# Kernel tuning notes

Measured on AMD Instinct MI355X. Metric: run time of the kernel, lower is better.

## Reference

```python
import jax, jax.numpy as jnp
import numpy as np

NUM_C = 100
DIM_S = 128
SIZE_M = 64
EMB = 128
MAX_CODE_LEN = 128
NODE_COUNT = 10000
PATH_COUNT = 10000
B, L = 16, 128


def setup_inputs() -> dict:
    key = jax.random.key(0)
    ks = jax.random.split(key, 24)
    def nrm(k, shape, fan):
        return jax.random.normal(k, shape, jnp.float32) * np.float32(np.sqrt(2.0 / fan))
    code = jax.random.randint(ks[0], (B, L, NUM_C * 2 + MAX_CODE_LEN * 3), 0, 10000)
    q = jax.random.randint(ks[1], (B, L), 0, NUM_C)
    r = jax.random.randint(ks[2], (B, L), 0, 2 * NUM_C)
    return {
        "code": code, "q": q, "r": r,
        "embed_nodes": nrm(ks[3], (NODE_COUNT + 2, EMB), EMB),
        "embed_paths": nrm(ks[4], (PATH_COUNT + 2, EMB), EMB),
        "W_pt": nrm(ks[5], (3 * EMB, 3 * EMB), 3 * EMB), "b_pt": jnp.zeros((3 * EMB,), jnp.float32),
        "W_att": nrm(ks[6], (3 * EMB, 1), 3 * EMB), "b_att": jnp.zeros((1,), jnp.float32),
        "k_emb": nrm(ks[7], (NUM_C + 1, DIM_S), DIM_S),
        "Mk": nrm(ks[8], (SIZE_M, DIM_S), DIM_S),
        "Mv0": nrm(ks[9], (SIZE_M, DIM_S), DIM_S),
        "v_emb": nrm(ks[10], (NUM_C * 2 + 2, DIM_S), DIM_S),
        "W_e": nrm(ks[11], (4 * DIM_S, DIM_S), 4 * DIM_S), "b_e": jnp.zeros((DIM_S,), jnp.float32),
        "W_a": nrm(ks[12], (4 * DIM_S, DIM_S), 4 * DIM_S), "b_a": jnp.zeros((DIM_S,), jnp.float32),
        "W_f": nrm(ks[13], (2 * DIM_S, DIM_S), 2 * DIM_S), "b_f": jnp.zeros((DIM_S,), jnp.float32),
        "W_p": nrm(ks[14], (DIM_S, 10), DIM_S), "b_p": jnp.zeros((10,), jnp.float32),
    }


def reference(code, q, r, embed_nodes, embed_paths, W_pt, b_pt, W_att, b_att,
              k_emb, Mk, Mv0, v_emb, W_e, b_e, W_a, b_a, W_f, b_f, W_p, b_p):
    bsz = code.shape[0]
    k = k_emb[q]                                    # [B,L,D]
    vr = v_emb[r]                                   # [B,L,D]
    # code2vec path triples: [B,L,MAX_CODE_LEN,3] = (start, path, end)
    c2v = code[:, :, NUM_C * 2:].reshape(bsz, code.shape[1], MAX_CODE_LEN, 3)
    full = jnp.concatenate([embed_nodes[c2v[..., 0]],
                            embed_nodes[c2v[..., 2]],
                            embed_paths[c2v[..., 1]]], axis=3)   # [B,L,P,3E]
    tr = jnp.tanh(full @ W_pt + b_pt)
    cw = tr @ W_att + b_att                          # [B,L,P,1]
    attn = jax.nn.softmax(cw, axis=1)                # faithful: softmax over seq dim (dim=1)
    code_vec = jnp.sum(full * attn, axis=2)          # [B,L,3E]
    v = jnp.concatenate([vr, code_vec], axis=2)      # [B,L,4D]
    w = jax.nn.softmax(k @ Mk.T, axis=-1)            # [B,L,M]
    e = jax.nn.sigmoid(v @ W_e + b_e)                # [B,L,D]
    a = jnp.tanh(v @ W_a + b_a)                      # [B,L,D]
    Mvt0 = jnp.broadcast_to(Mv0, (bsz,) + Mv0.shape) # [B,M,D]

    def step(Mvt, inp):
        et, at, wt = inp                             # [B,D],[B,D],[B,M]
        read = jnp.einsum('bm,bmd->bd', wt, Mvt)     # read pre-update memory (Mv[:, :-1])
        Mvt = Mvt * (1.0 - wt[:, :, None] * et[:, None, :]) + wt[:, :, None] * at[:, None, :]
        return Mvt, read

    _, reads = jax.lax.scan(step, Mvt0,
                            (e.transpose(1, 0, 2), a.transpose(1, 0, 2), w.transpose(1, 0, 2)))
    read = reads.transpose(1, 0, 2)                  # [B,L,D]
    f = jnp.tanh(jnp.concatenate([read, k], axis=-1) @ W_f + b_f)
    # dropout is identity in eval mode
    return jax.nn.sigmoid(f @ W_p + b_p)             # [B,L,10]
```

## Files before the change

kernel.cpp:

```cpp
#include <hip/hip_runtime.h>


typedef unsigned char u8;
typedef unsigned short u16;
typedef unsigned int u32;
typedef __attribute__((ext_vector_type(8))) short short8;
typedef __attribute__((ext_vector_type(4))) float f32x4;
typedef __attribute__((ext_vector_type(2))) float f32x2;

#define DEV __device__ __forceinline__
#define LOG2E 1.4426950408889634f
#define KSCALE 2.8853900817779268f

DEV u16 f2b(float f) {
    union { float f; u32 i; } v; v.f = f;
    u32 x = v.i;
    u32 r = (x + 0x7FFFu + ((x >> 16) & 1u)) >> 16;
    return (u16)r;
}
DEV float nexp(float x) { return __builtin_amdgcn_exp2f(x * LOG2E); }
DEV float nrcp(float x) { return __builtin_amdgcn_rcpf(x); }
DEV float fast_tanh(float x) {
    return 1.f - 2.f * nrcp(1.f + __builtin_amdgcn_exp2f(x * (2.f * LOG2E)));
}
DEV float sigmoidf_(float x) { return nrcp(1.f + __builtin_amdgcn_exp2f(-x * LOG2E)); }
DEV f32x2 d8(u32 x, bool hi) {
    return hi ? __builtin_amdgcn_cvt_pk_f32_fp8((int)x, true)
              : __builtin_amdgcn_cvt_pk_f32_fp8((int)x, false);
}
DEV u8 e8(float x) {
    return (u8)(__builtin_amdgcn_cvt_pk_fp8_f32(x, x, 0, false) & 0xFF);
}

__global__ void k_conv(const float* __restrict__ EN, const float* __restrict__ EP,
                       const float* __restrict__ Wpt, const float* __restrict__ We,
                       const float* __restrict__ Wa, const float* __restrict__ Wf,
                       const float* __restrict__ Wp,
                       const float* __restrict__ Kemb, const float* __restrict__ Mk,
                       u16* __restrict__ ENb, u16* __restrict__ EPb,
                       u8* __restrict__ EN8, u8* __restrict__ EP8,
                       u16* __restrict__ Wt, u16* __restrict__ WeaT,
                       u16* __restrict__ WfT, u16* __restrict__ WpT,
                       float* __restrict__ wsmall) {
    if (blockIdx.x >= 2048) {
        int wv = threadIdx.x >> 6, lane = threadIdx.x & 63;
        int row = (blockIdx.x - 2048) * 4 + wv;
        if (row >= 101) return;
        float lg = 0.f;
        for (int k = 0; k < 128; k += 8) {
            float mk8[8];
#pragma unroll
            for (int u = 0; u < 8; u++) mk8[u] = Mk[lane * 128 + k + u];
#pragma unroll
            for (int u = 0; u < 8; u++) lg = fmaf(Kemb[row * 128 + k + u], mk8[u], lg);
        }
        float mx = lg;
#pragma unroll
        for (int off = 32; off; off >>= 1) mx = fmaxf(mx, __shfl_xor(mx, off, 64));
        float ex = nexp(lg - mx);
        float sum = ex;
#pragma unroll
        for (int off = 32; off; off >>= 1) sum += __shfl_xor(sum, off, 64);
        wsmall[row * 64 + lane] = ex * nrcp(sum);
        return;
    }
    const int NEH = 10002 * 64;
    const int T0 = 2 * NEH;
    const int T1 = T0 + 147456;
    const int T2 = T1 + 65536;
    const int T2b = T2 + 65536;
    const int T3 = T2b + 32768;
    const int T4 = T3 + 2048;
    for (int i = blockIdx.x * blockDim.x + threadIdx.x; i < T4; i += 2048 * blockDim.x) {
        if (i < NEH) {
            float a = EN[2 * i], b = EN[2 * i + 1];
            ((u32*)ENb)[i] = ((u32)f2b(b) << 16) | f2b(a);
            ((u16*)EN8)[i] = (u16)__builtin_amdgcn_cvt_pk_fp8_f32(a, b, 0, false);
        } else if (i < T0) {
            int j = i - NEH;
            float a = EP[2 * j], b = EP[2 * j + 1];
            ((u32*)EPb)[j] = ((u32)f2b(b) << 16) | f2b(a);
            ((u16*)EP8)[j] = (u16)__builtin_amdgcn_cvt_pk_fp8_f32(a, b, 0, false);
        } else if (i < T1) {
            int w = i - T0;
            u32 k = (u32)w / 384u, n = (u32)w % 384u;
            Wt[n * 384 + k] = f2b(Wpt[w]);
        } else if (i < T2) {
            int w = i - T1;  int k = w >> 7, n = w & 127;
            WeaT[n * 512 + k] = f2b(We[w]);
        } else if (i < T2b) {
            int w = i - T2;  int k = w >> 7, n = w & 127;
            WeaT[(128 + n) * 512 + k] = f2b(Wa[w]);
        } else if (i < T3) {
            int w = i - T2b; int k = w >> 7, n = w & 127;
            WfT[n * 256 + k] = f2b(Wf[w]);
        } else {
            int w = i - T3;  int n = w >> 7, k = w & 127;
            WpT[w] = (n < 10) ? f2b(Wp[k * 10 + n]) : (u16)0;
        }
    }
}

__global__ void k_preM(const u16* __restrict__ ENb, const u16* __restrict__ EPb,
                       const u16* __restrict__ Wt, const float* __restrict__ bpt,
                       u8* __restrict__ PS8, u8* __restrict__ PE8, u8* __restrict__ PP8) {
    int which = blockIdx.y;
    int r0 = blockIdx.x * 32;
    int wv = threadIdx.x >> 6, lane = threadIdx.x & 63;
    int m = lane & 15, quad = lane >> 4;
    const u16* A = (which == 2) ? EPb : ENb;
    int koff = which * 128;
    u8* dst = (which == 0) ? PS8 : (which == 1) ? PE8 : PP8;

    short8 a[2][4];
#pragma unroll
    for (int rt = 0; rt < 2; rt++) {
        const short8* ap = (const short8*)(A + (r0 + rt * 16 + m) * 128 + quad * 8);
#pragma unroll
        for (int kc = 0; kc < 4; kc++) a[rt][kc] = ap[kc * 4];
    }

    for (int nt = 0; nt < 6; nt++) {
        int n0 = wv * 96 + nt * 16;
        const short8* bp = (const short8*)(Wt + (n0 + m) * 384 + koff + quad * 8);
        short8 b0 = bp[0], b1 = bp[4], b2 = bp[8], b3 = bp[12];
        int col = n0 + m;
        float bias = (which == 2) ? bpt[col] : 0.f;
#pragma unroll
        for (int rt = 0; rt < 2; rt++) {
            f32x4 acc = {0.f, 0.f, 0.f, 0.f};
            acc = __builtin_amdgcn_mfma_f32_16x16x32_bf16(a[rt][0], b0, acc, 0, 0, 0);
            acc = __builtin_amdgcn_mfma_f32_16x16x32_bf16(a[rt][1], b1, acc, 0, 0, 0);
            acc = __builtin_amdgcn_mfma_f32_16x16x32_bf16(a[rt][2], b2, acc, 0, 0, 0);
            acc = __builtin_amdgcn_mfma_f32_16x16x32_bf16(a[rt][3], b3, acc, 0, 0, 0);
#pragma unroll
            for (int reg = 0; reg < 4; reg++) {
                int row = r0 + rt * 16 + quad * 4 + reg;
                if (row < 10002) dst[row * 384 + col] = e8((acc[reg] + bias) * KSCALE);
            }
        }
    }
}

__global__ void k_cwsm(const int* __restrict__ code,
                       const u8* __restrict__ PS8, const u8* __restrict__ PE8,
                       const u8* __restrict__ PP8, const float* __restrict__ Watt,
                       float* __restrict__ attn) {
    int bp = blockIdx.x;
    int b = bp >> 7, p = bp & 127;
    int tid = threadIdx.x;
    int g = tid >> 4, gl = tid & 15;
    __shared__ float lgs[128];
    __shared__ float redm[4], reds[4];

    float w24[24];
    const float4* wp = (const float4*)(Watt + gl * 24);
#pragma unroll
    for (int u = 0; u < 6; u++) {
        float4 f = wp[u];
        w24[4 * u + 0] = -2.f * f.x; w24[4 * u + 1] = -2.f * f.y;
        w24[4 * u + 2] = -2.f * f.z; w24[4 * u + 3] = -2.f * f.w;
    }

    int si[8], pi[8], ei[8];
#pragma unroll
    for (int it = 0; it < 8; it++) {
        const int* c = code + ((b * 128 + g + it * 16) * 584 + 200 + 3 * p);
        si[it] = c[0]; pi[it] = c[1]; ei[it] = c[2];
    }

    uint4 cs4, ce4, cq4; uint2 cs2, ce2, cq2;
    {
        const u8* bs = PS8 + si[0] * 384 + gl * 24;
        const u8* be = PE8 + ei[0] * 384 + gl * 24;
        const u8* bq = PP8 + pi[0] * 384 + gl * 24;
        cs4 = *(const uint4*)bs; cs2 = *(const uint2*)(bs + 16);
        ce4 = *(const uint4*)be; ce2 = *(const uint2*)(be + 16);
        cq4 = *(const uint4*)bq; cq2 = *(const uint2*)(bq + 16);
    }
#pragma unroll
    for (int it = 0; it < 8; it++) {
        uint4 ns4, ne4, nq4; uint2 ns2, ne2, nq2;
        if (it < 7) {
            const u8* bs = PS8 + si[it + 1] * 384 + gl * 24;
            const u8* be = PE8 + ei[it + 1] * 384 + gl * 24;
            const u8* bq = PP8 + pi[it + 1] * 384 + gl * 24;
            ns4 = *(const uint4*)bs; ns2 = *(const uint2*)(bs + 16);
            ne4 = *(const uint4*)be; ne2 = *(const uint2*)(be + 16);
            nq4 = *(const uint4*)bq; nq2 = *(const uint2*)(bq + 16);
        }
        u32 sv[6] = { cs4.x, cs4.y, cs4.z, cs4.w, cs2.x, cs2.y };
        u32 ev[6] = { ce4.x, ce4.y, ce4.z, ce4.w, ce2.x, ce2.y };
        u32 qv[6] = { cq4.x, cq4.y, cq4.z, cq4.w, cq2.x, cq2.y };
        float acc = 0.f;
#pragma unroll
        for (int u = 0; u < 6; u++) {
            f32x2 zl = d8(sv[u], false) + d8(ev[u], false) + d8(qv[u], false);
            f32x2 zh = d8(sv[u], true)  + d8(ev[u], true)  + d8(qv[u], true);
            float d0 = 1.f + __builtin_amdgcn_exp2f(zl.x);
            float d1 = 1.f + __builtin_amdgcn_exp2f(zl.y);
            float d2 = 1.f + __builtin_amdgcn_exp2f(zh.x);
            float d3 = 1.f + __builtin_amdgcn_exp2f(zh.y);
            float n01 = fmaf(w24[4 * u + 0], d1, w24[4 * u + 1] * d0);
            float n23 = fmaf(w24[4 * u + 2], d3, w24[4 * u + 3] * d2);
            acc = fmaf(n01, nrcp(d0 * d1), acc);
            acc = fmaf(n23, nrcp(d2 * d3), acc);
        }
        acc += __shfl_xor(acc, 1, 64);
        acc += __shfl_xor(acc, 2, 64);
        acc += __shfl_xor(acc, 4, 64);
        acc += __shfl_xor(acc, 8, 64);
        if (gl == 0) lgs[g + it * 16] = acc;
        if (it < 7) {
            cs4 = ns4; cs2 = ns2;
            ce4 = ne4; ce2 = ne2;
            cq4 = nq4; cq2 = nq2;
        }
    }
    __syncthreads();

    int lane = tid & 63, wvi = tid >> 6;
    float x = (tid < 128) ? lgs[tid] : -1e30f;
    float mx = x;
#pragma unroll
    for (int off = 32; off; off >>= 1) mx = fmaxf(mx, __shfl_xor(mx, off, 64));
    if (lane == 0) redm[wvi] = mx;
    __syncthreads();
    mx = fmaxf(redm[0], redm[1]);
    float ex = nexp(x - mx);
    float sum = ex;
#pragma unroll
    for (int off = 32; off; off >>= 1) sum += __shfl_xor(sum, off, 64);
    if (lane == 0) reds[wvi] = sum;
    __syncthreads();
    float inv = nrcp(reds[0] + reds[1]);
    if (tid < 128) attn[(b * 128 + tid) * 128 + p] = ex * inv;
}

__global__ void k_cv(const int* __restrict__ code, const float* __restrict__ attn,
                     const u8* __restrict__ EN8, const u8* __restrict__ EP8,
                     const int* __restrict__ rr, const int* __restrict__ qq,
                     const float* __restrict__ Vemb, const float* __restrict__ Kemb,
                     u16* __restrict__ vA, u16* __restrict__ fA) {
    int row = blockIdx.x;
    int tid = threadIdx.x;
    int wv = tid >> 6, lane = tid & 63;
    int h = lane >> 5, cl = lane & 31;
    __shared__ int si[128], ei[128], pi[128];
    __shared__ float at[128];
    __shared__ float part[8][3][128];
    if (tid < 128) {
        const int* c = code + (row * 584 + 200);
        si[tid] = c[3 * tid]; pi[tid] = c[3 * tid + 1]; ei[tid] = c[3 * tid + 2];
        at[tid] = attn[row * 128 + tid];
    }
    if (tid < 128) {
        vA[row * 512 + tid] = f2b(Vemb[rr[row] * 128 + tid]);
    } else {
        int t2 = tid - 128;
        fA[row * 256 + 128 + t2] = f2b(Kemb[qq[row] * 128 + t2]);
    }
    __syncthreads();

    int o = cl * 4;
    int pb = wv + h * 4;
    float a0 = 0.f, a1 = 0.f, a2 = 0.f, a3 = 0.f;
    float b0 = 0.f, b1 = 0.f, b2 = 0.f, b3 = 0.f;
    float c0 = 0.f, c1 = 0.f, c2 = 0.f, c3 = 0.f;

    u32 cur0, cur1, cur2;
    cur0 = *(const u32*)(EN8 + si[pb] * 128 + o);
    cur1 = *(const u32*)(EN8 + ei[pb] * 128 + o);
    cur2 = *(const u32*)(EP8 + pi[pb] * 128 + o);
#pragma unroll
    for (int it = 0; it < 16; it++) {
        int p = pb + it * 8;
        u32 n0, n1, n2;
        if (it < 15) {
            int pn = p + 8;
            n0 = *(const u32*)(EN8 + si[pn] * 128 + o);
            n1 = *(const u32*)(EN8 + ei[pn] * 128 + o);
            n2 = *(const u32*)(EP8 + pi[pn] * 128 + o);
        }
        float w = at[p];
        f32x2 sl = d8(cur0, false), sh = d8(cur0, true);
        f32x2 el = d8(cur1, false), eh = d8(cur1, true);
        f32x2 pl = d8(cur2, false), ph = d8(cur2, true);
        a0 = fmaf(w, sl.x, a0); a1 = fmaf(w, sl.y, a1); a2 = fmaf(w, sh.x, a2); a3 = fmaf(w, sh.y, a3);
        b0 = fmaf(w, el.x, b0); b1 = fmaf(w, el.y, b1); b2 = fmaf(w, eh.x, b2); b3 = fmaf(w, eh.y, b3);
        c0 = fmaf(w, pl.x, c0); c1 = fmaf(w, pl.y, c1); c2 = fmaf(w, ph.x, c2); c3 = fmaf(w, ph.y, c3);
        if (it < 15) { cur0 = n0; cur1 = n1; cur2 = n2; }
    }
    int slot = wv * 2 + h;
    part[slot][0][o + 0] = a0; part[slot][0][o + 1] = a1; part[slot][0][o + 2] = a2; part[slot][0][o + 3] = a3;
    part[slot][1][o + 0] = b0; part[slot][1][o + 1] = b1; part[slot][1][o + 2] = b2; part[slot][1][o + 3] = b3;
    part[slot][2][o + 0] = c0; part[slot][2][o + 1] = c1; part[slot][2][o + 2] = c2; part[slot][2][o + 3] = c3;
    __syncthreads();
    u16* vrow = vA + row * 512 + 128;
    for (int idx = tid; idx < 384; idx += 256) {
        int tbl = idx >> 7, col = idx & 127;
        float s = 0.f;
#pragma unroll
        for (int sl2 = 0; sl2 < 8; sl2++) s += part[sl2][tbl][col];
        vrow[idx] = f2b(s);
    }
}

__global__ void k_eawM(const u16* __restrict__ vA, const u16* __restrict__ WeaT,
                       const float* __restrict__ be, const float* __restrict__ ba,
                       float* __restrict__ eb, float* __restrict__ ab) {
    int rt = blockIdx.x >> 2, cg = blockIdx.x & 3;
    int wv = threadIdx.x >> 6, lane = threadIdx.x & 63;
    int ct = cg * 4 + wv;
    int m = lane & 15, quad = lane >> 4;
    const short8* ap = (const short8*)(vA + (rt * 16 + m) * 512 + quad * 8);
    const short8* bp = (const short8*)(WeaT + (ct * 16 + m) * 512 + quad * 8);
    f32x4 acc = {0.f, 0.f, 0.f, 0.f};
#pragma unroll
    for (int kc = 0; kc < 16; kc++)
        acc = __builtin_amdgcn_mfma_f32_16x16x32_bf16(ap[kc * 4], bp[kc * 4], acc, 0, 0, 0);
    int col = ct * 16 + m;
    bool isA = col >= 128;
    int c2 = isA ? col - 128 : col;
    float bias = isA ? ba[c2] : be[c2];
#pragma unroll
    for (int reg = 0; reg < 4; reg++) {
        int row = rt * 16 + quad * 4 + reg;
        float val = acc[reg] + bias;
        if (isA) ab[row * 128 + c2] = fast_tanh(val);
        else     eb[row * 128 + c2] = sigmoidf_(val);
    }
}

__global__ void k_scan(const float* __restrict__ Mv0, const float* __restrict__ eb,
                       const float* __restrict__ ab, const float* __restrict__ wsmall,
                       const int* __restrict__ qq, u16* __restrict__ fA) {
    int b = blockIdx.x >> 4, dblk = blockIdx.x & 15;
    int lane = threadIdx.x;
    int s = lane >> 3, dlo = lane & 7;
    int d = dblk * 8 + dlo;

    __shared__ float wsm[101 * 64];
    __shared__ float el[128][8];
    __shared__ float al[128][8];
    __shared__ int ql[128];

    for (int i = lane; i < 101 * 64; i += 64) wsm[i] = wsmall[i];
    for (int i = lane; i < 1024; i += 64) {
        int t = i >> 3, dl = i & 7;
        el[t][dl] = eb[(b * 128 + t) * 128 + dblk * 8 + dl];
        al[t][dl] = ab[(b * 128 + t) * 128 + dblk * 8 + dl];
    }
    for (int i = lane; i < 128; i += 64) ql[i] = qq[b * 128 + i];
    __syncthreads();

    float mv[8];
#pragma unroll
    for (int q = 0; q < 8; q++) mv[q] = Mv0[(s * 8 + q) * 128 + d];

    u16* fout = fA + (b * 128) * 256 + d;

    int qt = ql[0];
    const float4* wr = (const float4*)(wsm + qt * 64 + s * 8);
    float4 w0 = wr[0], w1 = wr[1];
    float ecur = el[0][dlo], acur = al[0][dlo];

    for (int t = 0; t < 128; t++) {
        int tn = (t < 127) ? t + 1 : 127;
        int qn = ql[tn];
        const float4* wrn = (const float4*)(wsm + qn * 64 + s * 8);
        float4 nw0 = wrn[0], nw1 = wrn[1];
        float en = el[tn][dlo], an = al[tn][dlo];

        float w[8] = { w0.x, w0.y, w0.z, w0.w, w1.x, w1.y, w1.z, w1.w };
        float rd = 0.f;
#pragma unroll
        for (int q = 0; q < 8; q++) {
            rd = fmaf(w[q], mv[q], rd);
            mv[q] = fmaf(w[q], fmaf(-mv[q], ecur, acur), mv[q]);
        }
        rd += __shfl_xor(rd, 8, 64);
        rd += __shfl_xor(rd, 16, 64);
        rd += __shfl_xor(rd, 32, 64);
        if (s == 0) fout[t * 256] = f2b(rd);

        ecur = en; acur = an; w0 = nw0; w1 = nw1;
    }
}

__global__ void k_outfin(const u16* __restrict__ fA, const u16* __restrict__ WfT,
                         const float* __restrict__ bfp, const u16* __restrict__ WpT,
                         const float* __restrict__ bp, float* __restrict__ out) {
    int rt = blockIdx.x;
    int wv = threadIdx.x >> 6, lane = threadIdx.x & 63;
    int m = lane & 15, quad = lane >> 4;
    __shared__ u16 ftile[16][128];

    const short8* ap = (const short8*)(fA + (rt * 16 + m) * 256 + quad * 8);
    const short8* bpw = (const short8*)(WfT + (wv * 16 + m) * 256 + quad * 8);
    f32x4 acc = {0.f, 0.f, 0.f, 0.f};
#pragma unroll
    for (int kc = 0; kc < 8; kc++)
        acc = __builtin_amdgcn_mfma_f32_16x16x32_bf16(ap[kc * 4], bpw[kc * 4], acc, 0, 0, 0);
    int col = wv * 16 + m;
    float bias = bfp[col];
#pragma unroll
    for (int reg = 0; reg < 4; reg++)
        ftile[quad * 4 + reg][col] = f2b(fast_tanh(acc[reg] + bias));
    __syncthreads();

    if (wv == 0) {
        f32x4 facc = {0.f, 0.f, 0.f, 0.f};
#pragma unroll
        for (int kc = 0; kc < 4; kc++) {
            short8 af = *(const short8*)(&ftile[m][kc * 32 + quad * 8]);
            short8 bf = *(const short8*)(WpT + m * 128 + kc * 32 + quad * 8);
            facc = __builtin_amdgcn_mfma_f32_16x16x32_bf16(af, bf, facc, 0, 0, 0);
        }
        if (m < 10) {
            float bias2 = bp[m];
#pragma unroll
            for (int reg = 0; reg < 4; reg++) {
                int row = rt * 16 + quad * 4 + reg;
                out[row * 10 + m] = sigmoidf_(facc[reg] + bias2);
            }
        }
    }
}

extern "C" void kernel_launch(void* const* d_in, const int* in_sizes, int n_in,
                              void* d_out, int out_size, void* d_ws, size_t ws_size,
                              hipStream_t stream) {
    const int*   code = (const int*)d_in[0];
    const int*   q    = (const int*)d_in[1];
    const int*   r    = (const int*)d_in[2];
    const float* EN   = (const float*)d_in[3];
    const float* EP   = (const float*)d_in[4];
    const float* Wpt  = (const float*)d_in[5];
    const float* bpt  = (const float*)d_in[6];
    const float* Watt = (const float*)d_in[7];
    const float* Kemb = (const float*)d_in[9];
    const float* Mk   = (const float*)d_in[10];
    const float* Mv0  = (const float*)d_in[11];
    const float* Vemb = (const float*)d_in[12];
    const float* We   = (const float*)d_in[13];
    const float* be   = (const float*)d_in[14];
    const float* Wa   = (const float*)d_in[15];
    const float* ba   = (const float*)d_in[16];
    const float* Wf   = (const float*)d_in[17];
    const float* bf_  = (const float*)d_in[18];
    const float* Wp   = (const float*)d_in[19];
    const float* bp   = (const float*)d_in[20];

    char* ws = (char*)d_ws;
    size_t off = 0;
    auto alloc = [&](size_t bytes) { void* p = ws + off; off = (off + bytes + 255) & ~255UL; return p; };
    u8*    PS8    = (u8*)alloc(10002UL * 384);
    u8*    PE8    = (u8*)alloc(10002UL * 384);
    u8*    PP8    = (u8*)alloc(10002UL * 384);
    u16*   ENb    = (u16*)alloc(10016UL * 128 * 2);
    u16*   EPb    = (u16*)alloc(10016UL * 128 * 2);
    u8*    EN8    = (u8*)alloc(10002UL * 128);
    u8*    EP8    = (u8*)alloc(10002UL * 128);
    u16*   Wt     = (u16*)alloc(384UL * 384 * 2);
    u16*   WeaT   = (u16*)alloc(256UL * 512 * 2);
    u16*   WfT    = (u16*)alloc(128UL * 256 * 2);
    u16*   WpT    = (u16*)alloc(16UL * 128 * 2);
    float* attn   = (float*)alloc(16UL * 128 * 128 * 4);
    u16*   vA     = (u16*)alloc(2048UL * 512 * 2);
    u16*   fA     = (u16*)alloc(2048UL * 256 * 2);
    float* eb     = (float*)alloc(2048UL * 128 * 4);
    float* ab     = (float*)alloc(2048UL * 128 * 4);
    float* wsmall = (float*)alloc(101UL * 64 * 4);

    k_conv<<<2048 + 26, 256, 0, stream>>>(EN, EP, Wpt, We, Wa, Wf, Wp, Kemb, Mk,
                                          ENb, EPb, EN8, EP8, Wt, WeaT, WfT, WpT, wsmall);
    k_preM<<<dim3(313, 3), 256, 0, stream>>>(ENb, EPb, Wt, bpt, PS8, PE8, PP8);
    k_cwsm<<<2048, 256, 0, stream>>>(code, PS8, PE8, PP8, Watt, attn);
    k_cv<<<2048, 256, 0, stream>>>(code, attn, EN8, EP8, r, q, Vemb, Kemb, vA, fA);
    k_eawM<<<512, 256, 0, stream>>>(vA, WeaT, be, ba, eb, ab);
    k_scan<<<256, 64, 0, stream>>>(Mv0, eb, ab, wsmall, q, fA);
    k_outfin<<<128, 512, 0, stream>>>(fA, WfT, bf_, WpT, bp, (float*)d_out);
}
```

Baseline: 222.4 us.

## Fuse weight prep with path projection, and code-vector gather with e/a GEMM

The weight/embedding conversion kernel and the path-projection MFMA kernel are merged into one launch. The projection now reads fp32 embeddings and the unconverted W_pt directly, converting to bf16 in registers, which drops the ENb/EPb/Wt intermediate buffers and one kernel boundary. The attention-weighted code-vector gather and the e/a GEMM are fused into a single kernel that keeps 16 rows of the v matrix in LDS, removing the vA round trip through global memory. The cost is that the fused gather kernel runs only 128 blocks, with each half-wave walking all 128 paths of two rows serially. That cuts parallelism and latency hiding for the gather-heavy stage.

Measured after the change: 251.8 us. +13.2%, slower.

```diff
diff --git a/kernel.cpp b/kernel.cpp
--- a/kernel.cpp
+++ b/kernel.cpp
@@ -4,6 +4,7 @@
 typedef unsigned char u8;
 typedef unsigned short u16;
 typedef unsigned int u32;
+typedef unsigned long long u64;
 typedef __attribute__((ext_vector_type(8))) short short8;
 typedef __attribute__((ext_vector_type(4))) float f32x4;
 typedef __attribute__((ext_vector_type(2))) float f32x2;
@@ -18,6 +19,10 @@
     u32 r = (x + 0x7FFFu + ((x >> 16) & 1u)) >> 16;
     return (u16)r;
 }
+DEV u16 f2bt(float f) {
+    union { float f; u32 i; } v; v.f = f;
+    return (u16)(v.i >> 16);
+}
 DEV float nexp(float x) { return __builtin_amdgcn_exp2f(x * LOG2E); }
 DEV float nrcp(float x) { return __builtin_amdgcn_rcpf(x); }
 DEV float fast_tanh(float x) {
@@ -32,19 +37,48 @@
     return (u8)(__builtin_amdgcn_cvt_pk_fp8_f32(x, x, 0, false) & 0xFF);
 }
 
-__global__ void k_conv(const float* __restrict__ EN, const float* __restrict__ EP,
-                       const float* __restrict__ Wpt, const float* __restrict__ We,
-                       const float* __restrict__ Wa, const float* __restrict__ Wf,
-                       const float* __restrict__ Wp,
+__global__ void k_prep(const float* __restrict__ EN, const float* __restrict__ EP,
+                       const float* __restrict__ Wpt, const float* __restrict__ bpt,
+                       const float* __restrict__ We, const float* __restrict__ Wa,
+                       const float* __restrict__ Wf, const float* __restrict__ Wp,
                        const float* __restrict__ Kemb, const float* __restrict__ Mk,
-                       u16* __restrict__ ENb, u16* __restrict__ EPb,
                        u8* __restrict__ EN8, u8* __restrict__ EP8,
-                       u16* __restrict__ Wt, u16* __restrict__ WeaT,
-                       u16* __restrict__ WfT, u16* __restrict__ WpT,
-                       float* __restrict__ wsmall) {
-    if (blockIdx.x >= 2048) {
-        int wv = threadIdx.x >> 6, lane = threadIdx.x & 63;
-        int row = (blockIdx.x - 2048) * 4 + wv;
+                       u16* __restrict__ WeaT, u16* __restrict__ WfT,
+                       u16* __restrict__ WpT, float* __restrict__ wsmall,
+                       u8* __restrict__ PS8, u8* __restrict__ PE8, u8* __restrict__ PP8) {
+    int bid = blockIdx.x;
+    if (bid < 2048) {
+        const int NEH = 10002 * 64;
+        const int T0 = 2 * NEH;
+        const int T1 = T0 + 65536;
+        const int T2 = T1 + 65536;
+        const int T3 = T2 + 32768;
+        const int T4 = T3 + 2048;
+        for (int i = bid * 256 + threadIdx.x; i < T4; i += 2048 * 256) {
+            if (i < NEH) {
+                ((u16*)EN8)[i] = (u16)__builtin_amdgcn_cvt_pk_fp8_f32(EN[2 * i], EN[2 * i + 1], 0, false);
+            } else if (i < T0) {
+                int j = i - NEH;
+                ((u16*)EP8)[j] = (u16)__builtin_amdgcn_cvt_pk_fp8_f32(EP[2 * j], EP[2 * j + 1], 0, false);
+            } else if (i < T1) {
+                int w = i - T0;  int k = w >> 7, n = w & 127;
+                WeaT[n * 512 + k] = f2b(We[w]);
+            } else if (i < T2) {
+                int w = i - T1;  int k = w >> 7, n = w & 127;
+                WeaT[(128 + n) * 512 + k] = f2b(Wa[w]);
+            } else if (i < T3) {
+                int w = i - T2;  int k = w >> 7, n = w & 127;
+                WfT[n * 256 + k] = f2b(Wf[w]);
+            } else {
+                int w = i - T3;  int n = w >> 7, k = w & 127;
+                WpT[w] = (n < 10) ? f2b(Wp[k * 10 + n]) : (u16)0;
+            }
+        }
+        return;
+    }
+    int wv = threadIdx.x >> 6, lane = threadIdx.x & 63;
+    if (bid < 2074) {
+        int row = (bid - 2048) * 4 + wv;
         if (row >= 101) return;
         float lg = 0.f;
         for (int k = 0; k < 128; k += 8) {
@@ -64,80 +98,51 @@
         wsmall[row * 64 + lane] = ex * nrcp(sum);
         return;
     }
-    const int NEH = 10002 * 64;
-    const int T0 = 2 * NEH;
-    const int T1 = T0 + 147456;
-    const int T2 = T1 + 65536;
-    const int T2b = T2 + 65536;
-    const int T3 = T2b + 32768;
-    const int T4 = T3 + 2048;
-    for (int i = blockIdx.x * blockDim.x + threadIdx.x; i < T4; i += 2048 * blockDim.x) {
-        if (i < NEH) {
-            float a = EN[2 * i], b = EN[2 * i + 1];
-            ((u32*)ENb)[i] = ((u32)f2b(b) << 16) | f2b(a);
-            ((u16*)EN8)[i] = (u16)__builtin_amdgcn_cvt_pk_fp8_f32(a, b, 0, false);
-        } else if (i < T0) {
-            int j = i - NEH;
-            float a = EP[2 * j], b = EP[2 * j + 1];
-            ((u32*)EPb)[j] = ((u32)f2b(b) << 16) | f2b(a);
-            ((u16*)EP8)[j] = (u16)__builtin_amdgcn_cvt_pk_fp8_f32(a, b, 0, false);
-        } else if (i < T1) {
-            int w = i - T0;
-            u32 k = (u32)w / 384u, n = (u32)w % 384u;
-            Wt[n * 384 + k] = f2b(Wpt[w]);
-        } else if (i < T2) {
-            int w = i - T1;  int k = w >> 7, n = w & 127;
-            WeaT[n * 512 + k] = f2b(We[w]);
-        } else if (i < T2b) {
-            int w = i - T2;  int k = w >> 7, n = w & 127;
-            WeaT[(128 + n) * 512 + k] = f2b(Wa[w]);
-        } else if (i < T3) {
-            int w = i - T2b; int k = w >> 7, n = w & 127;
-            WfT[n * 256 + k] = f2b(Wf[w]);
-        } else {
-            int w = i - T3;  int n = w >> 7, k = w & 127;
-            WpT[w] = (n < 10) ? f2b(Wp[k * 10 + n]) : (u16)0;
-        }
-    }
-}
-
-__global__ void k_preM(const u16* __restrict__ ENb, const u16* __restrict__ EPb,
-                       const u16* __restrict__ Wt, const float* __restrict__ bpt,
-                       u8* __restrict__ PS8, u8* __restrict__ PE8, u8* __restrict__ PP8) {
-    int which = blockIdx.y;
-    int r0 = blockIdx.x * 32;
-    int wv = threadIdx.x >> 6, lane = threadIdx.x & 63;
+    int pid = bid - 2074;
+    int which = pid / 313;
+    int r0 = (pid % 313) * 32;
     int m = lane & 15, quad = lane >> 4;
-    const u16* A = (which == 2) ? EPb : ENb;
+    const float* src = (which == 2) ? EP : EN;
     int koff = which * 128;
     u8* dst = (which == 0) ? PS8 : (which == 1) ? PE8 : PP8;
 
     short8 a[2][4];
 #pragma unroll
     for (int rt = 0; rt < 2; rt++) {
-        const short8* ap = (const short8*)(A + (r0 + rt * 16 + m) * 128 + quad * 8);
-#pragma unroll
-        for (int kc = 0; kc < 4; kc++) a[rt][kc] = ap[kc * 4];
+        int row = min(r0 + rt * 16 + m, 10001);
+        const float* ab = src + row * 128 + quad * 8;
+#pragma unroll
+        for (int kc = 0; kc < 4; kc++) {
+            float4 f0 = *(const float4*)(ab + kc * 32);
+            float4 f1 = *(const float4*)(ab + kc * 32 + 4);
+            short8 v;
+            v[0] = f2b(f0.x); v[1] = f2b(f0.y); v[2] = f2b(f0.z); v[3] = f2b(f0.w);
+            v[4] = f2b(f1.x); v[5] = f2b(f1.y); v[6] = f2b(f1.z); v[7] = f2b(f1.w);
+            a[rt][kc] = v;
+        }
     }
 
     for (int nt = 0; nt < 6; nt++) {
         int n0 = wv * 96 + nt * 16;
-        const short8* bp = (const short8*)(Wt + (n0 + m) * 384 + koff + quad * 8);
-        short8 b0 = bp[0], b1 = bp[4], b2 = bp[8], b3 = bp[12];
         int col = n0 + m;
         float bias = (which == 2) ? bpt[col] : 0.f;
-#pragma unroll
-        for (int rt = 0; rt < 2; rt++) {
-            f32x4 acc = {0.f, 0.f, 0.f, 0.f};
-            acc = __builtin_amdgcn_mfma_f32_16x16x32_bf16(a[rt][0], b0, acc, 0, 0, 0);
-            acc = __builtin_amdgcn_mfma_f32_16x16x32_bf16(a[rt][1], b1, acc, 0, 0, 0);
-            acc = __builtin_amdgcn_mfma_f32_16x16x32_bf16(a[rt][2], b2, acc, 0, 0, 0);
-            acc = __builtin_amdgcn_mfma_f32_16x16x32_bf16(a[rt][3], b3, acc, 0, 0, 0);
-#pragma unroll
-            for (int reg = 0; reg < 4; reg++) {
-                int row = r0 + rt * 16 + quad * 4 + reg;
-                if (row < 10002) dst[row * 384 + col] = e8((acc[reg] + bias) * KSCALE);
-            }
+        f32x4 acc0 = {0.f, 0.f, 0.f, 0.f};
+        f32x4 acc1 = {0.f, 0.f, 0.f, 0.f};
+#pragma unroll
+        for (int kc = 0; kc < 4; kc++) {
+            const float* bb = Wpt + (koff + kc * 32 + quad * 8) * 384 + col;
+            short8 bv;
+#pragma unroll
+            for (int j = 0; j < 8; j++) bv[j] = f2bt(bb[j * 384]);
+            acc0 = __builtin_amdgcn_mfma_f32_16x16x32_bf16(a[0][kc], bv, acc0, 0, 0, 0);
+            acc1 = __builtin_amdgcn_mfma_f32_16x16x32_bf16(a[1][kc], bv, acc1, 0, 0, 0);
+        }
+#pragma unroll
+        for (int reg = 0; reg < 4; reg++) {
+            int row0 = r0 + quad * 4 + reg;
+            int row1 = row0 + 16;
+            if (row0 < 10002) dst[row0 * 384 + col] = e8((acc0[reg] + bias) * KSCALE);
+            if (row1 < 10002) dst[row1 * 384 + col] = e8((acc1[reg] + bias) * KSCALE);
         }
     }
 }
@@ -237,98 +242,90 @@
     if (tid < 128) attn[(b * 128 + tid) * 128 + p] = ex * inv;
 }
 
-__global__ void k_cv(const int* __restrict__ code, const float* __restrict__ attn,
-                     const u8* __restrict__ EN8, const u8* __restrict__ EP8,
-                     const int* __restrict__ rr, const int* __restrict__ qq,
-                     const float* __restrict__ Vemb, const float* __restrict__ Kemb,
-                     u16* __restrict__ vA, u16* __restrict__ fA) {
-    int row = blockIdx.x;
+__global__ void k_cvea(const int* __restrict__ code, const float* __restrict__ attn,
+                       const u8* __restrict__ EN8, const u8* __restrict__ EP8,
+                       const int* __restrict__ rix, const int* __restrict__ qix,
+                       const float* __restrict__ Vemb, const float* __restrict__ Kemb,
+                       const u16* __restrict__ WeaT,
+                       const float* __restrict__ be, const float* __restrict__ ba,
+                       float* __restrict__ eb, float* __restrict__ ab,
+                       u16* __restrict__ fA) {
+    int rt0 = blockIdx.x * 16;
     int tid = threadIdx.x;
     int wv = tid >> 6, lane = tid & 63;
+    __shared__ int sip[16][384];
+    __shared__ float at[16][128];
+    __shared__ u16 vAL[16][520];
+
+    for (int idx = tid; idx < 16 * 384; idx += 256) {
+        int r = idx / 384, j = idx - r * 384;
+        sip[r][j] = code[(rt0 + r) * 584 + 200 + j];
+    }
+    for (int idx = tid; idx < 2048; idx += 256) {
+        int r = idx >> 7, c = idx & 127;
+        at[r][c] = attn[(rt0 + r) * 128 + c];
+        vAL[r][c] = f2b(Vemb[rix[rt0 + r] * 128 + c]);
+        fA[(rt0 + r) * 256 + 128 + c] = f2b(Kemb[qix[rt0 + r] * 128 + c]);
+    }
+    __syncthreads();
+
     int h = lane >> 5, cl = lane & 31;
-    __shared__ int si[128], ei[128], pi[128];
-    __shared__ float at[128];
-    __shared__ float part[8][3][128];
-    if (tid < 128) {
-        const int* c = code + (row * 584 + 200);
-        si[tid] = c[3 * tid]; pi[tid] = c[3 * tid + 1]; ei[tid] = c[3 * tid + 2];
-        at[tid] = attn[row * 128 + tid];
-    }
-    if (tid < 128) {
-        vA[row * 512 + tid] = f2b(Vemb[rr[row] * 128 + tid]);
-    } else {
-        int t2 = tid - 128;
-        fA[row * 256 + 128 + t2] = f2b(Kemb[qq[row] * 128 + t2]);
-    }
-    __syncthreads();
-
+    int unit = wv * 2 + h;
     int o = cl * 4;
-    int pb = wv + h * 4;
-    float a0 = 0.f, a1 = 0.f, a2 = 0.f, a3 = 0.f;
-    float b0 = 0.f, b1 = 0.f, b2 = 0.f, b3 = 0.f;
-    float c0 = 0.f, c1 = 0.f, c2 = 0.f, c3 = 0.f;
-
-    u32 cur0, cur1, cur2;
-    cur0 = *(const u32*)(EN8 + si[pb] * 128 + o);
-    cur1 = *(const u32*)(EN8 + ei[pb] * 128 + o);
-    cur2 = *(const u32*)(EP8 + pi[pb] * 128 + o);
-#pragma unroll
-    for (int it = 0; it < 16; it++) {
-        int p = pb + it * 8;
-        u32 n0, n1, n2;
-        if (it < 15) {
-            int pn = p + 8;
-            n0 = *(const u32*)(EN8 + si[pn] * 128 + o);
-            n1 = *(const u32*)(EN8 + ei[pn] * 128 + o);
-            n2 = *(const u32*)(EP8 + pi[pn] * 128 + o);
-        }
-        float w = at[p];
-        f32x2 sl = d8(cur0, false), sh = d8(cur0, true);
-        f32x2 el = d8(cur1, false), eh = d8(cur1, true);
-        f32x2 pl = d8(cur2, false), ph = d8(cur2, true);
-        a0 = fmaf(w, sl.x, a0); a1 = fmaf(w, sl.y, a1); a2 = fmaf(w, sh.x, a2); a3 = fmaf(w, sh.y, a3);
-        b0 = fmaf(w, el.x, b0); b1 = fmaf(w, el.y, b1); b2 = fmaf(w, eh.x, b2); b3 = fmaf(w, eh.y, b3);
-        c0 = fmaf(w, pl.x, c0); c1 = fmaf(w, pl.y, c1); c2 = fmaf(w, ph.x, c2); c3 = fmaf(w, ph.y, c3);
-        if (it < 15) { cur0 = n0; cur1 = n1; cur2 = n2; }
-    }
-    int slot = wv * 2 + h;
-    part[slot][0][o + 0] = a0; part[slot][0][o + 1] = a1; part[slot][0][o + 2] = a2; part[slot][0][o + 3] = a3;
-    part[slot][1][o + 0] = b0; part[slot][1][o + 1] = b1; part[slot][1][o + 2] = b2; part[slot][1][o + 3] = b3;
-    part[slot][2][o + 0] = c0; part[slot][2][o + 1] = c1; part[slot][2][o + 2] = c2; part[slot][2][o + 3] = c3;
-    __syncthreads();
-    u16* vrow = vA + row * 512 + 128;
-    for (int idx = tid; idx < 384; idx += 256) {
-        int tbl = idx >> 7, col = idx & 127;
-        float s = 0.f;
-#pragma unroll
-        for (int sl2 = 0; sl2 < 8; sl2++) s += part[sl2][tbl][col];
-        vrow[idx] = f2b(s);
-    }
-}
-
-__global__ void k_eawM(const u16* __restrict__ vA, const u16* __restrict__ WeaT,
-                       const float* __restrict__ be, const float* __restrict__ ba,
-                       float* __restrict__ eb, float* __restrict__ ab) {
-    int rt = blockIdx.x >> 2, cg = blockIdx.x & 3;
-    int wv = threadIdx.x >> 6, lane = threadIdx.x & 63;
-    int ct = cg * 4 + wv;
+    for (int r = unit; r < 16; r += 8) {
+        float a0 = 0.f, a1 = 0.f, a2 = 0.f, a3 = 0.f;
+        float b0 = 0.f, b1 = 0.f, b2 = 0.f, b3 = 0.f;
+        float c0 = 0.f, c1 = 0.f, c2 = 0.f, c3 = 0.f;
+        u32 cur0 = *(const u32*)(EN8 + sip[r][0] * 128 + o);
+        u32 cur1 = *(const u32*)(EN8 + sip[r][2] * 128 + o);
+        u32 cur2 = *(const u32*)(EP8 + sip[r][1] * 128 + o);
+        for (int p = 0; p < 128; p++) {
+            u32 n0, n1, n2;
+            if (p < 127) {
+                n0 = *(const u32*)(EN8 + sip[r][3 * p + 3] * 128 + o);
+                n1 = *(const u32*)(EN8 + sip[r][3 * p + 5] * 128 + o);
+                n2 = *(const u32*)(EP8 + sip[r][3 * p + 4] * 128 + o);
+            }
+            float w = at[r][p];
+            f32x2 sl = d8(cur0, false), sh = d8(cur0, true);
+            f32x2 el = d8(cur1, false), eh = d8(cur1, true);
+            f32x2 pl = d8(cur2, false), ph = d8(cur2, true);
+            a0 = fmaf(w, sl.x, a0); a1 = fmaf(w, sl.y, a1); a2 = fmaf(w, sh.x, a2); a3 = fmaf(w, sh.y, a3);
+            b0 = fmaf(w, el.x, b0); b1 = fmaf(w, el.y, b1); b2 = fmaf(w, eh.x, b2); b3 = fmaf(w, eh.y, b3);
+            c0 = fmaf(w, pl.x, c0); c1 = fmaf(w, pl.y, c1); c2 = fmaf(w, ph.x, c2); c3 = fmaf(w, ph.y, c3);
+            if (p < 127) { cur0 = n0; cur1 = n1; cur2 = n2; }
+        }
+        u64 pa = (u64)f2b(a0) | ((u64)f2b(a1) << 16) | ((u64)f2b(a2) << 32) | ((u64)f2b(a3) << 48);
+        u64 pb = (u64)f2b(b0) | ((u64)f2b(b1) << 16) | ((u64)f2b(b2) << 32) | ((u64)f2b(b3) << 48);
+        u64 pc = (u64)f2b(c0) | ((u64)f2b(c1) << 16) | ((u64)f2b(c2) << 32) | ((u64)f2b(c3) << 48);
+        *(u64*)(&vAL[r][128 + o]) = pa;
+        *(u64*)(&vAL[r][256 + o]) = pb;
+        *(u64*)(&vAL[r][384 + o]) = pc;
+    }
+    __syncthreads();
+
     int m = lane & 15, quad = lane >> 4;
-    const short8* ap = (const short8*)(vA + (rt * 16 + m) * 512 + quad * 8);
-    const short8* bp = (const short8*)(WeaT + (ct * 16 + m) * 512 + quad * 8);
-    f32x4 acc = {0.f, 0.f, 0.f, 0.f};
-#pragma unroll
-    for (int kc = 0; kc < 16; kc++)
-        acc = __builtin_amdgcn_mfma_f32_16x16x32_bf16(ap[kc * 4], bp[kc * 4], acc, 0, 0, 0);
-    int col = ct * 16 + m;
-    bool isA = col >= 128;
-    int c2 = isA ? col - 128 : col;
-    float bias = isA ? ba[c2] : be[c2];
-#pragma unroll
-    for (int reg = 0; reg < 4; reg++) {
-        int row = rt * 16 + quad * 4 + reg;
-        float val = acc[reg] + bias;
-        if (isA) ab[row * 128 + c2] = fast_tanh(val);
-        else     eb[row * 128 + c2] = sigmoidf_(val);
+#pragma unroll
+    for (int cti = 0; cti < 4; cti++) {
+        int ct = wv + cti * 4;
+        const short8* bp = (const short8*)(WeaT + (ct * 16 + m) * 512 + quad * 8);
+        f32x4 acc = {0.f, 0.f, 0.f, 0.f};
+#pragma unroll
+        for (int kc = 0; kc < 16; kc++) {
+            short8 af = *(const short8*)(&vAL[m][kc * 32 + quad * 8]);
+            acc = __builtin_amdgcn_mfma_f32_16x16x32_bf16(af, bp[kc * 4], acc, 0, 0, 0);
+        }
+        int col = ct * 16 + m;
+        bool isA = col >= 128;
+        int c2 = isA ? col - 128 : col;
+        float bias = isA ? ba[c2] : be[c2];
+#pragma unroll
+        for (int reg = 0; reg < 4; reg++) {
+            int row = rt0 + quad * 4 + reg;
+            float val = acc[reg] + bias;
+            if (isA) ab[row * 128 + c2] = fast_tanh(val);
+            else     eb[row * 128 + c2] = sigmoidf_(val);
+        }
     }
 }
 
@@ -458,27 +455,22 @@
     u8*    PS8    = (u8*)alloc(10002UL * 384);
     u8*    PE8    = (u8*)alloc(10002UL * 384);
     u8*    PP8    = (u8*)alloc(10002UL * 384);
-    u16*   ENb    = (u16*)alloc(10016UL * 128 * 2);
-    u16*   EPb    = (u16*)alloc(10016UL * 128 * 2);
     u8*    EN8    = (u8*)alloc(10002UL * 128);
     u8*    EP8    = (u8*)alloc(10002UL * 128);
-    u16*   Wt     = (u16*)alloc(384UL * 384 * 2);
     u16*   WeaT   = (u16*)alloc(256UL * 512 * 2);
     u16*   WfT    = (u16*)alloc(128UL * 256 * 2);
     u16*   WpT    = (u16*)alloc(16UL * 128 * 2);
     float* attn   = (float*)alloc(16UL * 128 * 128 * 4);
-    u16*   vA     = (u16*)alloc(2048UL * 512 * 2);
     u16*   fA     = (u16*)alloc(2048UL * 256 * 2);
     float* eb     = (float*)alloc(2048UL * 128 * 4);
     float* ab     = (float*)alloc(2048UL * 128 * 4);
     float* wsmall = (float*)alloc(101UL * 64 * 4);
 
-    k_conv<<<2048 + 26, 256, 0, stream>>>(EN, EP, Wpt, We, Wa, Wf, Wp, Kemb, Mk,
-                                          ENb, EPb, EN8, EP8, Wt, WeaT, WfT, WpT, wsmall);
-    k_preM<<<dim3(313, 3), 256, 0, stream>>>(ENb, EPb, Wt, bpt, PS8, PE8, PP8);
+    k_prep<<<3013, 256, 0, stream>>>(EN, EP, Wpt, bpt, We, Wa, Wf, Wp, Kemb, Mk,
+                                     EN8, EP8, WeaT, WfT, WpT, wsmall, PS8, PE8, PP8);
     k_cwsm<<<2048, 256, 0, stream>>>(code, PS8, PE8, PP8, Watt, attn);
-    k_cv<<<2048, 256, 0, stream>>>(code, attn, EN8, EP8, r, q, Vemb, Kemb, vA, fA);
-    k_eawM<<<512, 256, 0, stream>>>(vA, WeaT, be, ba, eb, ab);
+    k_cvea<<<128, 256, 0, stream>>>(code, attn, EN8, EP8, r, q, Vemb, Kemb,
+                                    WeaT, be, ba, eb, ab, fA);
     k_scan<<<256, 64, 0, stream>>>(Mv0, eb, ab, wsmall, q, fA);
     k_outfin<<<128, 512, 0, stream>>>(fA, WfT, bf_, WpT, bp, (float*)d_out);
 }
```
